# Kernel optimization log

Hardware: AMD Instinct MI355X
Metric: run time of the kernel (lower is better)

The kernel has to match this reference:

```python
import jax, jax.numpy as jnp
import numpy as np

C = 4          # number of classes (cloud-organization dataset has 4)
EMPTY = 1.0    # IoU value when a class is absent from both pred and label


def setup_inputs() -> dict:
    key = jax.random.key(0)
    k1, k2 = jax.random.split(key)
    shape = (16, 1024, 1024)
    # preds are hard class predictions (stored as float, integer-valued)
    preds = jax.random.randint(k1, shape, 0, C).astype(jnp.float32)
    labels = jax.random.randint(k2, shape, 0, C).astype(jnp.int32)
    return {"preds": preds, "labels": labels}


def reference(preds, labels):
    # Vectorized form of the per-class loop:
    #   intersection_i = ((label == i) & (pred == i)).sum()
    #   union_i        = ((label == i) | (pred == i)).sum()   (ignore=None)
    cls = jnp.arange(C)                      # [C]
    pm = preds[..., None] == cls             # [B,H,W,C] bool
    lm = labels[..., None] == cls            # [B,H,W,C] bool
    inter = jnp.sum(pm & lm, axis=(0, 1, 2)).astype(jnp.float32)  # [C]
    union = jnp.sum(pm | lm, axis=(0, 1, 2)).astype(jnp.float32)  # [C]
    ious = jnp.where(union == 0, EMPTY, inter / jnp.where(union == 0, 1.0, union))
    ious_pct = 100.0 * ious                  # matches 100 * np.array(ious)
    return 1.0 - ious_pct                    # forward returns 1 - iou, shape [C]
```

## Files before the change

kernel.cpp:

```cpp
#include <hip/hip_runtime.h>


#define NCLS 4
#define NCNT (3 * NCLS)

__global__ __launch_bounds__(256) void iou_count_kernel(
    const float4* __restrict__ preds,
    const int4*   __restrict__ labels,
    unsigned int* __restrict__ partials,
    int n4)
{
    unsigned int acc_i = 0, acc_p = 0, acc_l = 0;

    const int tid    = blockIdx.x * blockDim.x + threadIdx.x;
    const int stride = gridDim.x * blockDim.x;

    auto proc = [&](float pf, int lv) {
        const int      ip = (int)pf;
        const unsigned tp = 1u << (ip << 3);
        const unsigned tl = 1u << (lv << 3);
        acc_p += tp;
        acc_l += tl;
        acc_i += (ip == lv) ? tl : 0u;
    };
    auto acc4 = [&](const float4 p, const int4 l) {
        proc(p.x, l.x); proc(p.y, l.y); proc(p.z, l.z); proc(p.w, l.w);
    };

    int idx = tid;
    for (; idx + stride < n4; idx += 2 * stride) {
        const float4 p0 = preds[idx];
        const float4 p1 = preds[idx + stride];
        const int4   l0 = labels[idx];
        const int4   l1 = labels[idx + stride];
        acc4(p0, l0);
        acc4(p1, l1);
    }
    for (; idx < n4; idx += stride)
        acc4(preds[idx], labels[idx]);

    unsigned pk[6];
    pk[0] = acc_i & 0x00FF00FFu; pk[1] = (acc_i >> 8) & 0x00FF00FFu;
    pk[2] = acc_p & 0x00FF00FFu; pk[3] = (acc_p >> 8) & 0x00FF00FFu;
    pk[4] = acc_l & 0x00FF00FFu; pk[5] = (acc_l >> 8) & 0x00FF00FFu;

#pragma unroll
    for (int k = 0; k < 6; ++k) {
#pragma unroll
        for (int off = 32; off > 0; off >>= 1)
            pk[k] += __shfl_down(pk[k], off);
    }

    __shared__ unsigned int s[4][6];
    const int wave = threadIdx.x >> 6;
    if ((threadIdx.x & 63) == 0) {
#pragma unroll
        for (int k = 0; k < 6; ++k) s[wave][k] = pk[k];
    }
    __syncthreads();

    if (threadIdx.x < 6) {
        const int k = threadIdx.x;
        const unsigned tot = s[0][k] + s[1][k] + s[2][k] + s[3][k];
        const int g = k >> 1, r = k & 1;
        partials[(g * NCLS + r)     * gridDim.x + blockIdx.x] = tot & 0xFFFFu;
        partials[(g * NCLS + r + 2) * gridDim.x + blockIdx.x] = tot >> 16;
    }
}

__global__ __launch_bounds__(768) void iou_reduce_kernel(
    const unsigned int* __restrict__ partials,
    float* __restrict__ out,
    int nblk)
{
    __shared__ unsigned int tot[NCNT];
    const int w    = threadIdx.x >> 6;
    const int lane = threadIdx.x & 63;

    if (w < NCNT) {
        unsigned int sum = 0;
        const unsigned int* row = partials + (size_t)w * nblk;
        for (int k = lane; k < nblk; k += 64)
            sum += row[k];
#pragma unroll
        for (int off = 32; off > 0; off >>= 1)
            sum += __shfl_down(sum, off);
        if (lane == 0) tot[w] = sum;
    }
    __syncthreads();

    if (threadIdx.x < NCLS) {
        const int c = threadIdx.x;
        const float inter = (float)tot[c];
        const float uni   = (float)tot[NCLS + c] + (float)tot[2 * NCLS + c]
                            - (float)tot[c];
        const float iou   = (uni == 0.0f) ? 1.0f : (inter / uni);
        out[c] = 1.0f - 100.0f * iou;
    }
}

extern "C" void kernel_launch(void* const* d_in, const int* in_sizes, int n_in,
                              void* d_out, int out_size, void* d_ws, size_t ws_size,
                              hipStream_t stream) {
    const float4* preds  = (const float4*)d_in[0];
    const int4*   labels = (const int4*)d_in[1];
    unsigned int* partials = (unsigned int*)d_ws;
    float* out = (float*)d_out;

    const int n  = in_sizes[0];
    const int n4 = n / 4;

    int nblk = 1024;
    const int cap = (int)(ws_size / (NCNT * sizeof(unsigned int)));
    if (cap < nblk) nblk = cap;
    if (nblk < 1) nblk = 1;

    iou_count_kernel<<<nblk, 256, 0, stream>>>(preds, labels, partials, n4);
    iou_reduce_kernel<<<1, 768, 0, stream>>>(partials, out, nblk);
}
```

Baseline: 144.4 us.

## Stream inputs through LDS with an async global_load_lds multi-stage pipeline

Replaces direct vectorized global loads with `__builtin_amdgcn_global_load_lds` into an 8-deep per-wave LDS ring buffer. Explicit `s_waitcnt` on vmcnt and lgkmcnt gates each stage before it is consumed and refilled. The goal is to keep many memory requests in flight per wave and hide HBM latency in this bandwidth-bound counting reduction. It also halves the grid to 512 blocks and handles the tail in a single wave. The trade-off is 64KB of LDS per block, which limits occupancy, plus reliance on hand-encoded waitcnt values.

```diff
diff --git a/kernel.cpp b/kernel.cpp
--- a/kernel.cpp
+++ b/kernel.cpp
@@ -3,17 +3,38 @@
 
 #define NCLS 4
 #define NCNT (3 * NCLS)
+#define QD 8
+#define CHUNK 1024
+#define WPB 4
+
+typedef float vf4 __attribute__((ext_vector_type(4)));
+typedef int   vi4 __attribute__((ext_vector_type(4)));
+
+typedef const __attribute__((address_space(1))) void glb_cv;
+typedef __attribute__((address_space(3))) void lds_v;
+
+#define WAITCNT_VM14 0x0F7E
+#define WAITCNT_VM0  0x0F70
+#define WAITCNT_LGKM0 0xC07F
+#define CFENCE asm volatile("" ::: "memory")
 
 __global__ __launch_bounds__(256) void iou_count_kernel(
-    const float4* __restrict__ preds,
-    const int4*   __restrict__ labels,
+    const float* __restrict__ preds,
+    const int*   __restrict__ labels,
     unsigned int* __restrict__ partials,
-    int n4)
+    int n)
 {
+    __shared__ unsigned char smem[WPB * QD * 2 * CHUNK];
+
+    const int lane = threadIdx.x & 63;
+    const int wid  = threadIdx.x >> 6;
+    const int gw   = blockIdx.x * WPB + wid;
+    const int W    = gridDim.x * WPB;
+    const int nch  = n >> 8;
+
+    unsigned char* const base = smem + wid * (QD * 2 * CHUNK);
+
     unsigned int acc_i = 0, acc_p = 0, acc_l = 0;
-
-    const int tid    = blockIdx.x * blockDim.x + threadIdx.x;
-    const int stride = gridDim.x * blockDim.x;
 
     auto proc = [&](float pf, int lv) {
         const int      ip = (int)pf;
@@ -23,21 +44,44 @@
         acc_l += tl;
         acc_i += (ip == lv) ? tl : 0u;
     };
-    auto acc4 = [&](const float4 p, const int4 l) {
+
+    auto issue = [&](int k) {
+        const int slot = k & (QD - 1);
+        const size_t c = (size_t)(gw + k * W) * 256 + lane * 4;
+        __builtin_amdgcn_global_load_lds(
+            (glb_cv*)(preds + c),
+            (lds_v*)(base + slot * 2 * CHUNK), 16, 0, 0);
+        __builtin_amdgcn_global_load_lds(
+            (glb_cv*)(labels + c),
+            (lds_v*)(base + slot * 2 * CHUNK + CHUNK), 16, 0, 0);
+    };
+
+    auto consume = [&](int k) {
+        const int slot = k & (QD - 1);
+        const vf4 p = *(const vf4*)(base + slot * 2 * CHUNK + lane * 16);
+        const vi4 l = *(const vi4*)(base + slot * 2 * CHUNK + CHUNK + lane * 16);
         proc(p.x, l.x); proc(p.y, l.y); proc(p.z, l.z); proc(p.w, l.w);
     };
 
-    int idx = tid;
-    for (; idx + stride < n4; idx += 2 * stride) {
-        const float4 p0 = preds[idx];
-        const float4 p1 = preds[idx + stride];
-        const int4   l0 = labels[idx];
-        const int4   l1 = labels[idx + stride];
-        acc4(p0, l0);
-        acc4(p1, l1);
+    const int K = (gw < nch) ? ((nch - gw - 1) / W + 1) : 0;
+
+    const int pro = (K < QD) ? K : QD;
+    for (int k = 0; k < pro; ++k) issue(k);
+
+    int k = 0;
+    for (; k < K - QD; ++k) {
+        CFENCE; __builtin_amdgcn_s_waitcnt(WAITCNT_VM14); CFENCE;
+        consume(k);
+        CFENCE; __builtin_amdgcn_s_waitcnt(WAITCNT_LGKM0); CFENCE;
+        issue(k + QD);
     }
-    for (; idx < n4; idx += stride)
-        acc4(preds[idx], labels[idx]);
+    CFENCE; __builtin_amdgcn_s_waitcnt(WAITCNT_VM0); CFENCE;
+    for (; k < K; ++k) consume(k);
+
+    if (blockIdx.x == 0 && wid == 0) {
+        for (int e = nch * 256 + lane; e < n; e += 64)
+            proc(preds[e], labels[e]);
+    }
 
     unsigned pk[6];
     pk[0] = acc_i & 0x00FF00FFu; pk[1] = (acc_i >> 8) & 0x00FF00FFu;
@@ -45,24 +89,23 @@
     pk[4] = acc_l & 0x00FF00FFu; pk[5] = (acc_l >> 8) & 0x00FF00FFu;
 
 #pragma unroll
-    for (int k = 0; k < 6; ++k) {
+    for (int j = 0; j < 6; ++j) {
 #pragma unroll
         for (int off = 32; off > 0; off >>= 1)
-            pk[k] += __shfl_down(pk[k], off);
+            pk[j] += __shfl_down(pk[j], off);
     }
 
-    __shared__ unsigned int s[4][6];
-    const int wave = threadIdx.x >> 6;
-    if ((threadIdx.x & 63) == 0) {
+    __shared__ unsigned int s[WPB][6];
+    if (lane == 0) {
 #pragma unroll
-        for (int k = 0; k < 6; ++k) s[wave][k] = pk[k];
+        for (int j = 0; j < 6; ++j) s[wid][j] = pk[j];
     }
     __syncthreads();
 
     if (threadIdx.x < 6) {
-        const int k = threadIdx.x;
-        const unsigned tot = s[0][k] + s[1][k] + s[2][k] + s[3][k];
-        const int g = k >> 1, r = k & 1;
+        const int j = threadIdx.x;
+        const unsigned tot = s[0][j] + s[1][j] + s[2][j] + s[3][j];
+        const int g = j >> 1, r = j & 1;
         partials[(g * NCLS + r)     * gridDim.x + blockIdx.x] = tot & 0xFFFFu;
         partials[(g * NCLS + r + 2) * gridDim.x + blockIdx.x] = tot >> 16;
     }
@@ -80,8 +123,8 @@
     if (w < NCNT) {
         unsigned int sum = 0;
         const unsigned int* row = partials + (size_t)w * nblk;
-        for (int k = lane; k < nblk; k += 64)
-            sum += row[k];
+        for (int i = lane; i < nblk; i += 64)
+            sum += row[i];
 #pragma unroll
         for (int off = 32; off > 0; off >>= 1)
             sum += __shfl_down(sum, off);
@@ -102,19 +145,18 @@
 extern "C" void kernel_launch(void* const* d_in, const int* in_sizes, int n_in,
                               void* d_out, int out_size, void* d_ws, size_t ws_size,
                               hipStream_t stream) {
-    const float4* preds  = (const float4*)d_in[0];
-    const int4*   labels = (const int4*)d_in[1];
+    const float* preds  = (const float*)d_in[0];
+    const int*   labels = (const int*)d_in[1];
     unsigned int* partials = (unsigned int*)d_ws;
     float* out = (float*)d_out;
 
-    const int n  = in_sizes[0];
-    const int n4 = n / 4;
+    const int n = in_sizes[0];
 
-    int nblk = 1024;
+    int nblk = 512;
     const int cap = (int)(ws_size / (NCNT * sizeof(unsigned int)));
     if (cap < nblk) nblk = cap;
     if (nblk < 1) nblk = 1;
 
-    iou_count_kernel<<<nblk, 256, 0, stream>>>(preds, labels, partials, n4);
+    iou_count_kernel<<<nblk, 256, 0, stream>>>(preds, labels, partials, n);
     iou_reduce_kernel<<<1, 768, 0, stream>>>(partials, out, nblk);
 }
```

Result: no change. 144.9 us (+0.4%).
